# Performance work log

Hardware: AMD Instinct MI355X
Metric: run time of the kernel (lower is better)

## Reference

```python
import jax, jax.numpy as jnp
import numpy as np

N_NODES = 40000
N_EDGES = 640000
D_IN = 128
D_HID = 128
D_OUT = 128
N_GRAPHS = 128


def setup_inputs() -> dict:
    key = jax.random.key(0)
    ks = jax.random.split(key, 12)
    x = jax.random.normal(ks[0], (N_NODES, D_IN), dtype=jnp.float32)
    edge_index = jax.random.randint(ks[1], (2, N_EDGES), 0, N_NODES, dtype=jnp.int64)
    batch = jnp.sort(jax.random.randint(ks[2], (N_NODES,), 0, N_GRAPHS, dtype=jnp.int64))
    def lin(k, fan_in, shape):
        s = 1.0 / np.sqrt(fan_in)
        return jax.random.uniform(k, shape, dtype=jnp.float32, minval=-s, maxval=s)
    return {
        "x": x, "edge_index": edge_index, "batch": batch,
        "W_rel0": lin(ks[3], D_IN, (D_IN, D_HID)), "b_rel0": lin(ks[4], D_IN, (D_HID,)), "W_root0": lin(ks[5], D_IN, (D_IN, D_HID)),
        "W_rel1": lin(ks[6], D_HID, (D_HID, D_HID)), "b_rel1": lin(ks[7], D_HID, (D_HID,)), "W_root1": lin(ks[8], D_HID, (D_HID, D_HID)),
        "W_rel2": lin(ks[9], D_HID, (D_HID, D_OUT)), "b_rel2": lin(ks[10], D_HID, (D_OUT,)), "W_root2": lin(ks[11], D_HID, (D_HID, D_OUT)),
    }


def graph_conv(x, src, dst, W_rel, b_rel, W_root):
    # PyG GraphConv: out_i = Lin_rel(sum_{j in N(i)} x_j) + Lin_root(x_i)
    agg = jax.ops.segment_sum(x[src], dst, num_segments=N_NODES)  # [N, F]
    return agg @ W_rel + b_rel + x @ W_root


def reference(x, edge_index, batch,
              W_rel0, b_rel0, W_root0,
              W_rel1, b_rel1, W_root1,
              W_rel2, b_rel2, W_root2):
    src, dst = edge_index[0], edge_index[1]
    h = graph_conv(x, src, dst, W_rel0, b_rel0, W_root0)
    h = jax.nn.relu(h)  # dropout is identity in eval mode
    h = graph_conv(h, src, dst, W_rel1, b_rel1, W_root1)
    h = jax.nn.relu(h)
    h = graph_conv(h, src, dst, W_rel2, b_rel2, W_root2)
    # global_max_pool over per-node graph ids -> [n_graphs, D_OUT]
    return jax.ops.segment_max(h, batch, num_segments=N_GRAPHS)
```

## Files before the change

### kernel.cpp

```cpp
#include <hip/hip_runtime.h>
#include <hip/hip_bf16.h>
#include <math.h>

#define N_NODES 40000
#define N_EDGES 640000
#define D 128
#define N_GRAPHS 128
#define SCAN_NBLK ((N_NODES + 255) / 256)
#define LDS_STRIDE 68

typedef __attribute__((ext_vector_type(8))) short bf16x8;
typedef __attribute__((ext_vector_type(4))) float f32x4;
typedef __attribute__((ext_vector_type(4))) unsigned int u32x4;

static __device__ __forceinline__ unsigned short f2b(float f) {
    unsigned int u = __float_as_uint(f);
    unsigned int r = (u + 0x7fffu + ((u >> 16) & 1u)) >> 16;
    return (unsigned short)r;
}
static __device__ __forceinline__ float blo(unsigned int u) {
    return __uint_as_float(u << 16);
}
static __device__ __forceinline__ float bhi(unsigned int u) {
    return __uint_as_float(u & 0xffff0000u);
}
static __device__ __forceinline__ unsigned int fkey(float x) {
    unsigned int b = __float_as_uint(x);
    return (b & 0x80000000u) ? ~b : (b | 0x80000000u);
}

__global__ void __launch_bounds__(256) k_init(
    const int* __restrict__ batch, int* __restrict__ counts,
    int* __restrict__ bounds,
    unsigned short* __restrict__ xb, unsigned short* __restrict__ hA,
    unsigned short* __restrict__ hB, unsigned int* __restrict__ outk) {
    int n = blockIdx.x * 256 + threadIdx.x;
    if (n < N_GRAPHS * D) outk[n] = 0x007FFFFFu;
    if (n < N_NODES) {
        counts[n] = 0;
        int b = batch[n];
        if (n == 0) {
            for (int g = 0; g <= b; ++g) bounds[g] = 0;
        } else {
            int pb = batch[n - 1];
            for (int g = pb + 1; g <= b; ++g) bounds[g] = n;
        }
        if (n == N_NODES - 1) {
            for (int g = b + 1; g <= N_GRAPHS; ++g) bounds[g] = N_NODES;
        }
    }
    if (blockIdx.x == SCAN_NBLK) {
        int t = threadIdx.x;
        if (t < 48) {
            int row = t >> 4, c = t & 15;
            unsigned short* p = (row == 0) ? xb : (row == 1) ? hA : hB;
            u32x4 z = {0u, 0u, 0u, 0u};
            ((u32x4*)(p + (size_t)N_NODES * D))[c] = z;
        }
    }
}

__global__ void __launch_bounds__(256) k_pack1(
    const int* __restrict__ ei, int* __restrict__ counts,
    const float* __restrict__ x, unsigned int* __restrict__ xb,
    const float* __restrict__ Wr0, const float* __restrict__ Wt0,
    const float* __restrict__ Wr1, const float* __restrict__ Wt1,
    const float* __restrict__ Wr2, const float* __restrict__ Wt2,
    unsigned short* __restrict__ WT) {
    int b = blockIdx.x;
    int t = threadIdx.x;
    if (b < 2500) {
        int e = b * 256 + t;
        atomicAdd(&counts[ei[N_EDGES + e]], 1);
    } else if (b < 5000) {
        int i = (b - 2500) * 256 + t;
        const f32x4* xv = (const f32x4*)x;
        f32x4 v0 = xv[i * 2], v1 = xv[i * 2 + 1];
        u32x4 o;
        o.x = ((unsigned int)f2b(v0.y) << 16) | f2b(v0.x);
        o.y = ((unsigned int)f2b(v0.w) << 16) | f2b(v0.z);
        o.z = ((unsigned int)f2b(v1.y) << 16) | f2b(v1.x);
        o.w = ((unsigned int)f2b(v1.w) << 16) | f2b(v1.z);
        ((u32x4*)xb)[i] = o;
    } else {
        int bw = b - 5000;
        int l = bw >> 7, c = bw & 127, k = t;
        const float* Wrel = (l == 0) ? Wr0 : (l == 1) ? Wr1 : Wr2;
        const float* Wroot = (l == 0) ? Wt0 : (l == 1) ? Wt1 : Wt2;
        float v = (k < D) ? Wrel[k * D + c] : Wroot[(k - D) * D + c];
        WT[(size_t)l * 128 * 256 + c * 256 + k] = f2b(v);
    }
}

__global__ void __launch_bounds__(256) k_scan1(const int* __restrict__ counts,
                                               int* __restrict__ local_pre,
                                               int* __restrict__ blocksums) {
    int t = threadIdx.x;
    int i = blockIdx.x * 256 + t;
    int lane = t & 63, wave = t >> 6;
    int v = (i < N_NODES) ? ((counts[i] + 15) & ~15) : 0;
    int incl = v;
#pragma unroll
    for (int off = 1; off < 64; off <<= 1) {
        int u = __shfl_up(incl, off);
        if (lane >= off) incl += u;
    }
    __shared__ int ws[4];
    if (lane == 63) ws[wave] = incl;
    __syncthreads();
    int base = 0;
    for (int w = 0; w < 4; ++w) {
        int s = ws[w];
        if (w < wave) base += s;
    }
    if (i < N_NODES) local_pre[i] = base + incl - v;
    if (t == 255) blocksums[blockIdx.x] = base + incl;
}

__global__ void __launch_bounds__(256) k_scan2(int* __restrict__ blocksums) {
    int t = threadIdx.x;
    int lane = t & 63, wave = t >> 6;
    int v = (t < SCAN_NBLK) ? blocksums[t] : 0;
    int incl = v;
#pragma unroll
    for (int off = 1; off < 64; off <<= 1) {
        int u = __shfl_up(incl, off);
        if (lane >= off) incl += u;
    }
    __shared__ int ws[4];
    if (lane == 63) ws[wave] = incl;
    __syncthreads();
    int base = 0;
    for (int w = 0; w < 4; ++w) {
        int s = ws[w];
        if (w < wave) base += s;
    }
    if (t < SCAN_NBLK) blocksums[t] = base + incl - v;
}

__global__ void __launch_bounds__(256) k_scan3(const int* __restrict__ local_pre,
                                               const int* __restrict__ blocksums,
                                               const int* __restrict__ counts,
                                               int* __restrict__ rp_pad,
                                               int* __restrict__ cursor,
                                               int* __restrict__ src_pad) {
    int i = blockIdx.x * 256 + threadIdx.x;
    if (i < N_NODES) {
        int rp = blocksums[blockIdx.x] + local_pre[i];
        rp_pad[i] = rp;
        cursor[i] = rp;
        int c = counts[i];
        int pc = (c + 15) & ~15;
        for (int j = rp + c; j < rp + pc; ++j) src_pad[j] = N_NODES;
        if (i == N_NODES - 1) rp_pad[N_NODES] = rp + pc;
    }
}

__global__ void k_scatter(const int* __restrict__ ei, int* __restrict__ cursor,
                          int* __restrict__ src_pad) {
    int e = blockIdx.x * blockDim.x + threadIdx.x;
    if (e < N_EDGES) {
        int d = ei[N_EDGES + e];
        int pos = atomicAdd(&cursor[d], 1);
        src_pad[pos] = ei[e];
    }
}

__global__ void __launch_bounds__(256) k_layer(
    const unsigned short* __restrict__ in,
    const int* __restrict__ rp_pad,
    const int* __restrict__ src_pad,
    const unsigned short* __restrict__ WT,
    const float* __restrict__ bias,
    unsigned short* __restrict__ out,
    const int* __restrict__ batch,
    unsigned int* __restrict__ outk) {
    __shared__ unsigned int aggLDS[16 * LDS_STRIDE];
    int tid = threadIdx.x;
    int w = tid >> 6;
    int lane = tid & 63;
    int q = lane >> 4;
    int c = lane & 15;
    int nl = w * 4 + q;
    int nodebase = blockIdx.x * 16;
    const u32x4* inv = (const u32x4*)in;

    int row = c, quad = q;
    int colbase = w * 32;
    const short* Xp = (const short*)(in + (nodebase + row) * D);
    const short* W0 = (const short*)(WT + (colbase + row) * 256);
    const short* W1 = (const short*)(WT + (colbase + 16 + row) * 256);
    bf16x8 xf[4], b0a[4], b1a[4];
#pragma unroll
    for (int t = 0; t < 4; ++t) {
        int k0 = t * 32 + quad * 8;
        xf[t] = *(const bf16x8*)(Xp + k0);
        b0a[t] = *(const bf16x8*)(W0 + k0);
        b1a[t] = *(const bf16x8*)(W1 + k0);
    }

    int s = rp_pad[nodebase + nl];
    int e = rp_pad[nodebase + nl + 1];
    const int4* sidx = (const int4*)(src_pad + s);
    int ntrips = (e - s) >> 4;

    float a0 = 0.f, a1 = 0.f, a2 = 0.f, a3 = 0.f;
    float a4 = 0.f, a5 = 0.f, a6 = 0.f, a7 = 0.f;

#define ACC8(v) do { \
        a0 += blo((v).x); a1 += bhi((v).x); \
        a2 += blo((v).y); a3 += bhi((v).y); \
        a4 += blo((v).z); a5 += bhi((v).z); \
        a6 += blo((v).w); a7 += bhi((v).w); } while (0)

    for (int t = 0; t < ntrips; ++t) {
        int4 ia = sidx[4 * t + 0];
        int4 ib = sidx[4 * t + 1];
        int4 ic = sidx[4 * t + 2];
        int4 id = sidx[4 * t + 3];
        u32x4 v0 = inv[ia.x * 16 + c];
        u32x4 v1 = inv[ia.y * 16 + c];
        u32x4 v2 = inv[ia.z * 16 + c];
        u32x4 v3 = inv[ia.w * 16 + c];
        u32x4 v4 = inv[ib.x * 16 + c];
        u32x4 v5 = inv[ib.y * 16 + c];
        u32x4 v6 = inv[ib.z * 16 + c];
        u32x4 v7 = inv[ib.w * 16 + c];
        u32x4 v8 = inv[ic.x * 16 + c];
        u32x4 v9 = inv[ic.y * 16 + c];
        u32x4 va = inv[ic.z * 16 + c];
        u32x4 vb = inv[ic.w * 16 + c];
        u32x4 vc = inv[id.x * 16 + c];
        u32x4 vd = inv[id.y * 16 + c];
        u32x4 ve = inv[id.z * 16 + c];
        u32x4 vf = inv[id.w * 16 + c];
        ACC8(v0); ACC8(v1); ACC8(v2); ACC8(v3);
        ACC8(v4); ACC8(v5); ACC8(v6); ACC8(v7);
        ACC8(v8); ACC8(v9); ACC8(va); ACC8(vb);
        ACC8(vc); ACC8(vd); ACC8(ve); ACC8(vf);
    }
#undef ACC8

    u32x4 o;
    o.x = ((unsigned int)f2b(a1) << 16) | f2b(a0);
    o.y = ((unsigned int)f2b(a3) << 16) | f2b(a2);
    o.z = ((unsigned int)f2b(a5) << 16) | f2b(a4);
    o.w = ((unsigned int)f2b(a7) << 16) | f2b(a6);
    *(u32x4*)&aggLDS[nl * LDS_STRIDE + c * 4] = o;
    __syncthreads();

    f32x4 acc0 = {0.f, 0.f, 0.f, 0.f};
    f32x4 acc1 = {0.f, 0.f, 0.f, 0.f};
    const unsigned int* Al = &aggLDS[row * LDS_STRIDE];

#pragma unroll
    for (int t = 0; t < 4; ++t) {
        bf16x8 af = *(const bf16x8*)(Al + t * 16 + quad * 4);
        acc0 = __builtin_amdgcn_mfma_f32_16x16x32_bf16(af, b0a[t], acc0, 0, 0, 0);
        acc1 = __builtin_amdgcn_mfma_f32_16x16x32_bf16(af, b1a[t], acc1, 0, 0, 0);
    }
#pragma unroll
    for (int t = 0; t < 4; ++t) {
        int k0 = t * 32 + quad * 8;
        bf16x8 b0 = *(const bf16x8*)(W0 + 128 + k0);
        bf16x8 b1 = *(const bf16x8*)(W1 + 128 + k0);
        acc0 = __builtin_amdgcn_mfma_f32_16x16x32_bf16(xf[t], b0, acc0, 0, 0, 0);
        acc1 = __builtin_amdgcn_mfma_f32_16x16x32_bf16(xf[t], b1, acc1, 0, 0, 0);
    }

    int c0 = colbase + row, c1 = c0 + 16;
    float bia0 = bias[c0], bia1 = bias[c1];
    float v0[4], v1[4];
#pragma unroll
    for (int r = 0; r < 4; ++r) { v0[r] = acc0[r] + bia0; v1[r] = acc1[r] + bia1; }

    if (outk == nullptr) {
#pragma unroll
        for (int r = 0; r < 4; ++r) {
            int n2 = nodebase + quad * 4 + r;
            out[n2 * D + c0] = f2b(fmaxf(v0[r], 0.f));
            out[n2 * D + c1] = f2b(fmaxf(v1[r], 0.f));
        }
    } else {
        int g0 = batch[nodebase];
        int g15 = batch[nodebase + 15];
        if (g0 == g15) {
            float m0 = fmaxf(fmaxf(v0[0], v0[1]), fmaxf(v0[2], v0[3]));
            float m1 = fmaxf(fmaxf(v1[0], v1[1]), fmaxf(v1[2], v1[3]));
            m0 = fmaxf(m0, __shfl_xor(m0, 16)); m0 = fmaxf(m0, __shfl_xor(m0, 32));
            m1 = fmaxf(m1, __shfl_xor(m1, 16)); m1 = fmaxf(m1, __shfl_xor(m1, 32));
            if (quad == 0) {
                atomicMax(&outk[g0 * D + c0], fkey(m0));
                atomicMax(&outk[g0 * D + c1], fkey(m1));
            }
        } else {
#pragma unroll
            for (int r = 0; r < 4; ++r) {
                int gg = batch[nodebase + quad * 4 + r];
                atomicMax(&outk[gg * D + c0], fkey(v0[r]));
                atomicMax(&outk[gg * D + c1], fkey(v1[r]));
            }
        }
    }
}

__global__ void k_unmap(unsigned int* __restrict__ outk) {
    int i = blockIdx.x * 256 + threadIdx.x;
    unsigned int k = outk[i];
    unsigned int b = (k & 0x80000000u) ? (k ^ 0x80000000u) : ~k;
    ((float*)outk)[i] = __uint_as_float(b);
}

extern "C" void kernel_launch(void* const* d_in, const int* in_sizes, int n_in,
                              void* d_out, int out_size, void* d_ws, size_t ws_size,
                              hipStream_t stream) {
    const float* x = (const float*)d_in[0];
    const int* ei = (const int*)d_in[1];
    const int* batch = (const int*)d_in[2];
    const float* Wrel[3]  = {(const float*)d_in[3], (const float*)d_in[6], (const float*)d_in[9]};
    const float* brel[3]  = {(const float*)d_in[4], (const float*)d_in[7], (const float*)d_in[10]};
    const float* Wroot[3] = {(const float*)d_in[5], (const float*)d_in[8], (const float*)d_in[11]};
    unsigned int* outk = (unsigned int*)d_out;

    char* ws = (char*)d_ws;
    size_t off = 0;
    auto alloc = [&](size_t bytes) -> void* {
        void* p = ws + off;
        off = (off + bytes + 255) & ~(size_t)255;
        return p;
    };
    unsigned short* xb  = (unsigned short*)alloc((size_t)(N_NODES + 1) * D * 2);
    unsigned short* hA  = (unsigned short*)alloc((size_t)(N_NODES + 1) * D * 2);
    unsigned short* hB  = (unsigned short*)alloc((size_t)(N_NODES + 1) * D * 2);
    unsigned short* WT  = (unsigned short*)alloc((size_t)3 * 128 * 256 * 2);
    int* rp_pad     = (int*)alloc((size_t)(N_NODES + 1) * 4);
    int* counts     = (int*)alloc((size_t)N_NODES * 4);
    int* cursor     = (int*)alloc((size_t)N_NODES * 4);
    int* src_pad    = (int*)alloc((size_t)(N_EDGES + 16 * N_NODES) * 4);
    int* bounds     = (int*)alloc((size_t)(N_GRAPHS + 1) * 4);
    int* local_pre  = (int*)alloc((size_t)N_NODES * 4);
    int* blocksums  = (int*)alloc((size_t)SCAN_NBLK * 4);

    k_init<<<SCAN_NBLK + 1, 256, 0, stream>>>(batch, counts, bounds, xb, hA, hB, outk);
    k_pack1<<<5384, 256, 0, stream>>>(ei, counts, x, (unsigned int*)xb,
                                      Wrel[0], Wroot[0], Wrel[1], Wroot[1],
                                      Wrel[2], Wroot[2], WT);
    k_scan1<<<SCAN_NBLK, 256, 0, stream>>>(counts, local_pre, blocksums);
    k_scan2<<<1, 256, 0, stream>>>(blocksums);
    k_scan3<<<SCAN_NBLK, 256, 0, stream>>>(local_pre, blocksums, counts,
                                           rp_pad, cursor, src_pad);
    k_scatter<<<(N_EDGES + 255) / 256, 256, 0, stream>>>(ei, cursor, src_pad);

    k_layer<<<N_NODES / 16, 256, 0, stream>>>(xb, rp_pad, src_pad, WT,
                                              brel[0], hA, batch, nullptr);
    k_layer<<<N_NODES / 16, 256, 0, stream>>>(hA, rp_pad, src_pad, WT + 128 * 256,
                                              brel[1], hB, batch, nullptr);
    k_layer<<<N_NODES / 16, 256, 0, stream>>>(hB, rp_pad, src_pad, WT + 2 * 128 * 256,
                                              brel[2], hB, batch, outk);

    k_unmap<<<N_GRAPHS * D / 256, 256, 0, stream>>>(outk);
}
```

Baseline: 276.1 us.

## Fold block-sum scan into scan3, drop unused bounds, defer weight loads in layer

```diff
diff --git a/kernel.cpp b/kernel.cpp
--- a/kernel.cpp
+++ b/kernel.cpp
@@ -31,24 +31,11 @@
 
 __global__ void __launch_bounds__(256) k_init(
     const int* __restrict__ batch, int* __restrict__ counts,
-    int* __restrict__ bounds,
     unsigned short* __restrict__ xb, unsigned short* __restrict__ hA,
     unsigned short* __restrict__ hB, unsigned int* __restrict__ outk) {
     int n = blockIdx.x * 256 + threadIdx.x;
     if (n < N_GRAPHS * D) outk[n] = 0x007FFFFFu;
-    if (n < N_NODES) {
-        counts[n] = 0;
-        int b = batch[n];
-        if (n == 0) {
-            for (int g = 0; g <= b; ++g) bounds[g] = 0;
-        } else {
-            int pb = batch[n - 1];
-            for (int g = pb + 1; g <= b; ++g) bounds[g] = n;
-        }
-        if (n == N_NODES - 1) {
-            for (int g = b + 1; g <= N_GRAPHS; ++g) bounds[g] = N_NODES;
-        }
-    }
+    if (n < N_NODES) counts[n] = 0;
     if (blockIdx.x == SCAN_NBLK) {
         int t = threadIdx.x;
         if (t < 48) {
@@ -117,36 +104,26 @@
     if (t == 255) blocksums[blockIdx.x] = base + incl;
 }
 
-__global__ void __launch_bounds__(256) k_scan2(int* __restrict__ blocksums) {
-    int t = threadIdx.x;
-    int lane = t & 63, wave = t >> 6;
-    int v = (t < SCAN_NBLK) ? blocksums[t] : 0;
-    int incl = v;
-#pragma unroll
-    for (int off = 1; off < 64; off <<= 1) {
-        int u = __shfl_up(incl, off);
-        if (lane >= off) incl += u;
-    }
-    __shared__ int ws[4];
-    if (lane == 63) ws[wave] = incl;
-    __syncthreads();
-    int base = 0;
-    for (int w = 0; w < 4; ++w) {
-        int s = ws[w];
-        if (w < wave) base += s;
-    }
-    if (t < SCAN_NBLK) blocksums[t] = base + incl - v;
-}
-
 __global__ void __launch_bounds__(256) k_scan3(const int* __restrict__ local_pre,
                                                const int* __restrict__ blocksums,
                                                const int* __restrict__ counts,
                                                int* __restrict__ rp_pad,
                                                int* __restrict__ cursor,
                                                int* __restrict__ src_pad) {
-    int i = blockIdx.x * 256 + threadIdx.x;
+    int t = threadIdx.x;
+    int lane = t & 63, wave = t >> 6;
+    int bid = blockIdx.x;
+    int v = (t < bid) ? blocksums[t] : 0;
+#pragma unroll
+    for (int off = 32; off >= 1; off >>= 1) v += __shfl_xor(v, off);
+    __shared__ int ws[4];
+    if (lane == 0) ws[wave] = v;
+    __syncthreads();
+    int base = ws[0] + ws[1] + ws[2] + ws[3];
+
+    int i = bid * 256 + t;
     if (i < N_NODES) {
-        int rp = blocksums[blockIdx.x] + local_pre[i];
+        int rp = base + local_pre[i];
         rp_pad[i] = rp;
         cursor[i] = rp;
         int c = counts[i];
@@ -184,20 +161,6 @@
     int nl = w * 4 + q;
     int nodebase = blockIdx.x * 16;
     const u32x4* inv = (const u32x4*)in;
-
-    int row = c, quad = q;
-    int colbase = w * 32;
-    const short* Xp = (const short*)(in + (nodebase + row) * D);
-    const short* W0 = (const short*)(WT + (colbase + row) * 256);
-    const short* W1 = (const short*)(WT + (colbase + 16 + row) * 256);
-    bf16x8 xf[4], b0a[4], b1a[4];
-#pragma unroll
-    for (int t = 0; t < 4; ++t) {
-        int k0 = t * 32 + quad * 8;
-        xf[t] = *(const bf16x8*)(Xp + k0);
-        b0a[t] = *(const bf16x8*)(W0 + k0);
-        b1a[t] = *(const bf16x8*)(W1 + k0);
-    }
 
     int s = rp_pad[nodebase + nl];
     int e = rp_pad[nodebase + nl + 1];
@@ -249,23 +212,34 @@
     *(u32x4*)&aggLDS[nl * LDS_STRIDE + c * 4] = o;
     __syncthreads();
 
+    int row = c, quad = q;
+    int colbase = w * 32;
+
     f32x4 acc0 = {0.f, 0.f, 0.f, 0.f};
     f32x4 acc1 = {0.f, 0.f, 0.f, 0.f};
+
     const unsigned int* Al = &aggLDS[row * LDS_STRIDE];
+    const short* Xp = (const short*)(in + (nodebase + row) * D);
+    const short* W0 = (const short*)(WT + (colbase + row) * 256);
+    const short* W1 = (const short*)(WT + (colbase + 16 + row) * 256);
 
 #pragma unroll
     for (int t = 0; t < 4; ++t) {
         bf16x8 af = *(const bf16x8*)(Al + t * 16 + quad * 4);
-        acc0 = __builtin_amdgcn_mfma_f32_16x16x32_bf16(af, b0a[t], acc0, 0, 0, 0);
-        acc1 = __builtin_amdgcn_mfma_f32_16x16x32_bf16(af, b1a[t], acc1, 0, 0, 0);
+        int k0 = t * 32 + quad * 8;
+        bf16x8 b0 = *(const bf16x8*)(W0 + k0);
+        bf16x8 b1 = *(const bf16x8*)(W1 + k0);
+        acc0 = __builtin_amdgcn_mfma_f32_16x16x32_bf16(af, b0, acc0, 0, 0, 0);
+        acc1 = __builtin_amdgcn_mfma_f32_16x16x32_bf16(af, b1, acc1, 0, 0, 0);
     }
 #pragma unroll
     for (int t = 0; t < 4; ++t) {
         int k0 = t * 32 + quad * 8;
+        bf16x8 xf = *(const bf16x8*)(Xp + k0);
         bf16x8 b0 = *(const bf16x8*)(W0 + 128 + k0);
         bf16x8 b1 = *(const bf16x8*)(W1 + 128 + k0);
-        acc0 = __builtin_amdgcn_mfma_f32_16x16x32_bf16(xf[t], b0, acc0, 0, 0, 0);
-        acc1 = __builtin_amdgcn_mfma_f32_16x16x32_bf16(xf[t], b1, acc1, 0, 0, 0);
+        acc0 = __builtin_amdgcn_mfma_f32_16x16x32_bf16(xf, b0, acc0, 0, 0, 0);
+        acc1 = __builtin_amdgcn_mfma_f32_16x16x32_bf16(xf, b1, acc1, 0, 0, 0);
     }
 
     int c0 = colbase + row, c1 = c0 + 16;
@@ -337,16 +311,14 @@
     int* counts     = (int*)alloc((size_t)N_NODES * 4);
     int* cursor     = (int*)alloc((size_t)N_NODES * 4);
     int* src_pad    = (int*)alloc((size_t)(N_EDGES + 16 * N_NODES) * 4);
-    int* bounds     = (int*)alloc((size_t)(N_GRAPHS + 1) * 4);
     int* local_pre  = (int*)alloc((size_t)N_NODES * 4);
     int* blocksums  = (int*)alloc((size_t)SCAN_NBLK * 4);
 
-    k_init<<<SCAN_NBLK + 1, 256, 0, stream>>>(batch, counts, bounds, xb, hA, hB, outk);
+    k_init<<<SCAN_NBLK + 1, 256, 0, stream>>>(batch, counts, xb, hA, hB, outk);
     k_pack1<<<5384, 256, 0, stream>>>(ei, counts, x, (unsigned int*)xb,
                                       Wrel[0], Wroot[0], Wrel[1], Wroot[1],
                                       Wrel[2], Wroot[2], WT);
     k_scan1<<<SCAN_NBLK, 256, 0, stream>>>(counts, local_pre, blocksums);
-    k_scan2<<<1, 256, 0, stream>>>(blocksums);
     k_scan3<<<SCAN_NBLK, 256, 0, stream>>>(local_pre, blocksums, counts,
                                            rp_pad, cursor, src_pad);
     k_scatter<<<(N_EDGES + 255) / 256, 256, 0, stream>>>(ei, cursor, src_pad);
```

Result: no change. 273.4 us (-1.0%).
